# Kernel tuning notes

Hardware: AMD Instinct MI355X
Metric: run time of the kernel (lower is better)

The kernel has to match this reference:

```python
import jax, jax.numpy as jnp
import numpy as np

SZ = 256          # image side
K = 4             # neighbors
NUM_CHANNELS = 8
CHUNK = 512       # query chunk for brute-force KNN
BIG = 1e10        # penalty added to squared distance of non-filled candidates


def _fill_channel(img, mask):
    """img: [SZ,SZ] float, mask: [SZ,SZ] bool. Returns filled [SZ,SZ].

    Faithful to TreeMultiRandom: filled pixels = mask nonzero; for every
    unfilled pixel take K nearest filled pixels (Euclidean on coords/SZ,
    i.e. norm_coord) and fill with sum(val_j * dist_j) / sum(dist_j)
    (NOTE: the original weights by distance, not inverse distance; kept as-is).
    Filled pixels keep their (masked) value.
    """
    N = SZ * SZ
    r = jnp.arange(SZ, dtype=jnp.float32) / SZ  # norm_coord
    gy, gx = jnp.meshgrid(r, r, indexing='ij')  # (row, col) like .nonzero()
    py = gy.reshape(N)
    px = gx.reshape(N)
    mflat = mask.reshape(N)
    vflat = (img * mask).reshape(N)  # holed image values
    penalty = jnp.where(mflat, 0.0, BIG).astype(jnp.float32)

    def chunk_fn(q):
        qy, qx = q  # each [CHUNK]
        # masked squared distances to all candidates: [CHUNK, N]
        d2 = (qy[:, None] - py[None, :]) ** 2 + (qx[:, None] - px[None, :]) ** 2 \
             + penalty[None, :]
        neg, idx = jax.lax.top_k(-d2, K)          # K smallest distances
        dist = jnp.sqrt(jnp.maximum(-neg, 0.0))   # [CHUNK, K] (KDTree returns L2)
        v = vflat[idx]                            # gather neighbor values
        return jnp.sum(v * dist, axis=1) / jnp.sum(dist, axis=1)

    qys = py.reshape(-1, CHUNK)
    qxs = px.reshape(-1, CHUNK)
    vals = jax.lax.map(chunk_fn, (qys, qxs)).reshape(N)
    # unfilled pixels get interpolated vals; filled keep holed value
    return jnp.where(mflat, vflat, vals).reshape(SZ, SZ)


def reference(coded, lookup_table):
    img = coded[0, 0]  # [SZ, SZ]
    chans = [_fill_channel(img, lookup_table == c)
             for c in range(1, NUM_CHANNELS + 1)]
    return jnp.stack(chans)[None]  # [1, NUM_CHANNELS, SZ, SZ]


def setup_inputs() -> dict:
    key = jax.random.key(0)
    k1, k2 = jax.random.split(key)
    coded = jax.random.normal(k1, (1, 1, SZ, SZ), dtype=jnp.float32)
    # values in 1..NUM_CHANNELS so every channel has a nonempty filled set
    lookup_table = jax.random.randint(k2, (SZ, SZ), 1, NUM_CHANNELS + 1,
                                      dtype=jnp.int32)
    return {"coded": coded, "lookup_table": lookup_table}
```

## Files before the change

### kernel.cpp

```cpp
#include <hip/hip_runtime.h>
#include <math.h>

#define SZ 256
#define KNN 4
#define NUM_CHANNELS 8
#define R 7
#define WROWS (2 * R + 1)
#define RSTRIDE 6

typedef unsigned long long u64;
typedef unsigned int u32;

__device__ __forceinline__ void ins4(u32 key, u32& k0, u32& k1,
                                     u32& k2, u32& k3) {
    u32 m;
    m = (k2 > key) ? k2 : key;  k3 = (k3 < m) ? k3 : m;
    m = (k1 > key) ? k1 : key;  k2 = (k2 < m) ? k2 : m;
    m = (k0 > key) ? k0 : key;  k1 = (k1 < m) ? k1 : m;
    k0 = (k0 < key) ? k0 : key;
}

__device__ __forceinline__ void ins4_64(u64 key, u64& k0, u64& k1,
                                        u64& k2, u64& k3) {
    if (key < k3) {
        u64 m;
        m = (k2 > key) ? k2 : key;  k3 = (k3 < m) ? k3 : m;
        m = (k1 > key) ? k1 : key;  k2 = (k2 < m) ? k2 : m;
        m = (k0 > key) ? k0 : key;  k1 = (k1 < m) ? k1 : m;
        k0 = (k0 < key) ? k0 : key;
    }
}

__global__ __launch_bounds__(256) void knn_fill(
    const float* __restrict__ img,
    const int*   __restrict__ lut,
    float*       __restrict__ out)
{
    __shared__ u64 win[WROWS * RSTRIDE];

    const int x    = threadIdx.x;
    const int y    = blockIdx.x;
    const int ch   = blockIdx.y;
    const int c    = ch + 1;
    const int lane = x & 63;
    const int w64  = x >> 6;

    int y0 = y - R;
    if (y0 < 0) y0 = 0;
    if (y0 > SZ - WROWS) y0 = SZ - WROWS;

    if (x < WROWS * 2) win[(x >> 1) * RSTRIDE + (x & 1) * 5] = 0;

    #pragma unroll
    for (int rr = 0; rr < WROWS; ++rr) {
        const int v = lut[(y0 + rr) * SZ + x];
        const u64 bal = __ballot(v == c);
        if (lane == 0) win[rr * RSTRIDE + 1 + w64] = bal;
    }
    __syncthreads();

    const int pix = y * SZ + x;
    float* outc = out + (size_t)ch * (SZ * SZ);

    const int rrc = y - y0;
    if ((win[rrc * RSTRIDE + 1 + (x >> 6)] >> (x & 63)) & 1ull) {
        outc[pix] = img[pix];
        return;
    }

    u32 k0 = ~0u, k1 = ~0u, k2 = ~0u, k3 = ~0u;

    const int base = x - R + 64;
    const int wrd  = base >> 6;
    const int sh   = base & 63;

    #pragma unroll
    for (int rr = 0; rr < WROWS; ++rr) {
        const u64 lo = win[rr * RSTRIDE + wrd];
        const u64 hi = win[rr * RSTRIDE + wrd + 1];
        u32 w = (u32)((u64)(((((unsigned __int128)hi) << 64) | lo) >> sh))
                & ((1u << WROWS) - 1);
        const int dy   = y0 + rr - y;
        const int dy2  = dy * dy;
        const int rowx = (y0 + rr) * SZ + x;
        while (w) {
            const int b = __builtin_ctz(w);
            w &= w - 1;
            const int dx  = b - R;
            const u32 d2  = (u32)(dy2 + dx * dx);
            const u32 key = (d2 << 16) | (u32)(rowx + dx);
            ins4(key, k0, k1, k2, k3);
        }
    }

    u64 ks[KNN];
    const u32 in_d2 = k3 >> 16;
    if (in_d2 < (u32)((R + 1) * (R + 1))) {
        ks[0] = k0; ks[1] = k1; ks[2] = k2; ks[3] = k3;
    } else {
        const u64 cap = (in_d2 != 0xFFFFu) ? (u64)in_d2 : 65535ull;
        u64 q0 = ~0ull, q1 = ~0ull, q2 = ~0ull, q3 = ~0ull;
        for (int ady = 0; ady < SZ; ++ady) {
            u64 cur = q3 >> 16;
            if (cap < cur) cur = cap;
            const u64 a2 = (u64)(ady * ady);
            if (a2 > cur) break;
            int Rx;
            const u64 bound = cur - a2;
            if (bound >= 65025ull) Rx = SZ - 1;
            else Rx = (int)sqrtf((float)bound) + 1;
            int xs = x - Rx; if (xs < 0) xs = 0;
            int xe = x + Rx; if (xe > SZ - 1) xe = SZ - 1;
            for (int s = 0; s < 2; ++s) {
                if (s && ady == 0) continue;
                const int yy = s ? y + ady : y - ady;
                if (yy < 0 || yy > SZ - 1) continue;
                const int rb = yy * SZ;
                for (int xx = xs; xx <= xe; ++xx) {
                    if (lut[rb + xx] == c) {
                        const int dxx = xx - x;
                        const u64 d2 = a2 + (u64)(dxx * dxx);
                        ins4_64((d2 << 16) | (u32)(rb + xx), q0, q1, q2, q3);
                    }
                }
            }
        }
        ks[0] = q0; ks[1] = q1; ks[2] = q2; ks[3] = q3;
    }

    float num = 0.0f, den = 0.0f;
    #pragma unroll
    for (int i = 0; i < KNN; ++i) {
        const int idx = (int)(ks[i] & 0xFFFFull);
        const int d2i = (int)(ks[i] >> 16);
        const float dist = sqrtf((float)d2i * (1.0f / 65536.0f));
        num += img[idx] * dist;
        den += dist;
    }
    outc[pix] = num / den;
}

extern "C" void kernel_launch(void* const* d_in, const int* in_sizes, int n_in,
                              void* d_out, int out_size, void* d_ws, size_t ws_size,
                              hipStream_t stream) {
    const float* img = (const float*)d_in[0];
    const int*   lut = (const int*)d_in[1];
    float*       out = (float*)d_out;

    knn_fill<<<dim3(SZ, NUM_CHANNELS), dim3(256), 0, stream>>>(img, lut, out);
}
```

Baseline: 88.77 us.

## Widen shared bitmask window and scan fallback KNN with bitmask popcount iteration

Extends the shared-memory ballot bitmask window from 15 to 33 rows and rewrites the fallback search to walk set bits of the bitmask rather than reading the lookup table from global memory pixel by pixel. A third tier, the original global-memory scan, is kept for pixels whose fourth neighbor lies beyond radius 16. The aim is to cut global loads and the per-pixel loop cost for sparse channels. In exchange every block does more than twice as many ballot loads up front, even when the fallback never runs.

```diff
diff --git a/kernel.cpp b/kernel.cpp
--- a/kernel.cpp
+++ b/kernel.cpp
@@ -6,6 +6,8 @@
 #define NUM_CHANNELS 8
 #define R 7
 #define WROWS (2 * R + 1)
+#define FR 16
+#define FROWS (2 * FR + 1)
 #define RSTRIDE 6
 
 typedef unsigned long long u64;
@@ -36,7 +38,7 @@
     const int*   __restrict__ lut,
     float*       __restrict__ out)
 {
-    __shared__ u64 win[WROWS * RSTRIDE];
+    __shared__ u64 win[FROWS * RSTRIDE];
 
     const int x    = threadIdx.x;
     const int y    = blockIdx.x;
@@ -45,15 +47,19 @@
     const int lane = x & 63;
     const int w64  = x >> 6;
 
-    int y0 = y - R;
-    if (y0 < 0) y0 = 0;
-    if (y0 > SZ - WROWS) y0 = SZ - WROWS;
+    int y0b = y - FR;
+    if (y0b < 0) y0b = 0;
+    if (y0b > SZ - FROWS) y0b = SZ - FROWS;
+    int y0m = y - R;
+    if (y0m < 0) y0m = 0;
+    if (y0m > SZ - WROWS) y0m = SZ - WROWS;
+    const int rstart = y0m - y0b;
 
-    if (x < WROWS * 2) win[(x >> 1) * RSTRIDE + (x & 1) * 5] = 0;
+    if (x < FROWS * 2) win[(x >> 1) * RSTRIDE + (x & 1) * 5] = 0;
 
     #pragma unroll
-    for (int rr = 0; rr < WROWS; ++rr) {
-        const int v = lut[(y0 + rr) * SZ + x];
+    for (int rr = 0; rr < FROWS; ++rr) {
+        const int v = lut[(y0b + rr) * SZ + x];
         const u64 bal = __ballot(v == c);
         if (lane == 0) win[rr * RSTRIDE + 1 + w64] = bal;
     }
@@ -62,8 +68,7 @@
     const int pix = y * SZ + x;
     float* outc = out + (size_t)ch * (SZ * SZ);
 
-    const int rrc = y - y0;
-    if ((win[rrc * RSTRIDE + 1 + (x >> 6)] >> (x & 63)) & 1ull) {
+    if ((win[(y - y0b) * RSTRIDE + 1 + (x >> 6)] >> (x & 63)) & 1ull) {
         outc[pix] = img[pix];
         return;
     }
@@ -76,13 +81,14 @@
 
     #pragma unroll
     for (int rr = 0; rr < WROWS; ++rr) {
-        const u64 lo = win[rr * RSTRIDE + wrd];
-        const u64 hi = win[rr * RSTRIDE + wrd + 1];
+        const int rr2 = rstart + rr;
+        const u64 lo = win[rr2 * RSTRIDE + wrd];
+        const u64 hi = win[rr2 * RSTRIDE + wrd + 1];
         u32 w = (u32)((u64)(((((unsigned __int128)hi) << 64) | lo) >> sh))
                 & ((1u << WROWS) - 1);
-        const int dy   = y0 + rr - y;
+        const int dy   = y0m + rr - y;
         const int dy2  = dy * dy;
-        const int rowx = (y0 + rr) * SZ + x;
+        const int rowx = (y0m + rr) * SZ + x;
         while (w) {
             const int b = __builtin_ctz(w);
             w &= w - 1;
@@ -98,34 +104,76 @@
     if (in_d2 < (u32)((R + 1) * (R + 1))) {
         ks[0] = k0; ks[1] = k1; ks[2] = k2; ks[3] = k3;
     } else {
-        const u64 cap = (in_d2 != 0xFFFFu) ? (u64)in_d2 : 65535ull;
-        u64 q0 = ~0ull, q1 = ~0ull, q2 = ~0ull, q3 = ~0ull;
-        for (int ady = 0; ady < SZ; ++ady) {
-            u64 cur = q3 >> 16;
+        const u32 cap = in_d2;
+        u32 q0 = ~0u, q1 = ~0u, q2 = ~0u, q3 = ~0u;
+        for (int ady = 0; ady < FROWS; ++ady) {
+            u32 cur = q3 >> 16;
             if (cap < cur) cur = cap;
-            const u64 a2 = (u64)(ady * ady);
+            const u32 a2 = (u32)(ady * ady);
             if (a2 > cur) break;
-            int Rx;
-            const u64 bound = cur - a2;
-            if (bound >= 65025ull) Rx = SZ - 1;
-            else Rx = (int)sqrtf((float)bound) + 1;
+            const u32 bound = cur - a2;
+            int Rx = (bound >= 65025u) ? (SZ - 1)
+                                       : ((int)sqrtf((float)bound) + 1);
             int xs = x - Rx; if (xs < 0) xs = 0;
             int xe = x + Rx; if (xe > SZ - 1) xe = SZ - 1;
+            const int jxs = xs >> 6, jxe = xe >> 6;
+            const u64 mlo = (~0ull) << (xs & 63);
+            const u64 mhi = (~0ull) >> (63 - (xe & 63));
+            #pragma unroll
             for (int s = 0; s < 2; ++s) {
                 if (s && ady == 0) continue;
                 const int yy = s ? y + ady : y - ady;
-                if (yy < 0 || yy > SZ - 1) continue;
+                const int rr2 = yy - y0b;
+                if (rr2 < 0 || rr2 >= FROWS) continue;
                 const int rb = yy * SZ;
-                for (int xx = xs; xx <= xe; ++xx) {
-                    if (lut[rb + xx] == c) {
+                const u64* rw = &win[rr2 * RSTRIDE + 1];
+                for (int j = jxs; j <= jxe; ++j) {
+                    u64 w = rw[j];
+                    if (j == jxs) w &= mlo;
+                    if (j == jxe) w &= mhi;
+                    while (w) {
+                        const int b = __builtin_ctzll(w);
+                        w &= w - 1;
+                        const int xx = (j << 6) + b;
                         const int dxx = xx - x;
-                        const u64 d2 = a2 + (u64)(dxx * dxx);
-                        ins4_64((d2 << 16) | (u32)(rb + xx), q0, q1, q2, q3);
+                        const u32 d2 = a2 + (u32)(dxx * dxx);
+                        ins4((d2 << 16) | (u32)(rb + xx), q0, q1, q2, q3);
                     }
                 }
             }
         }
-        ks[0] = q0; ks[1] = q1; ks[2] = q2; ks[3] = q3;
+        if ((q3 >> 16) < 289u) {
+            ks[0] = q0; ks[1] = q1; ks[2] = q2; ks[3] = q3;
+        } else {
+            const u64 cap2 = (q3 != ~0u) ? (u64)(q3 >> 16) : (~0ull >> 16);
+            u64 t0 = ~0ull, t1 = ~0ull, t2 = ~0ull, t3 = ~0ull;
+            for (int ady = 0; ady < SZ; ++ady) {
+                u64 cur = t3 >> 16;
+                if (cap2 < cur) cur = cap2;
+                const u64 a2 = (u64)(ady * ady);
+                if (a2 > cur) break;
+                const u64 bound = cur - a2;
+                int Rx = (bound >= 65025ull) ? (SZ - 1)
+                                             : ((int)sqrtf((float)bound) + 1);
+                int xs = x - Rx; if (xs < 0) xs = 0;
+                int xe = x + Rx; if (xe > SZ - 1) xe = SZ - 1;
+                for (int s = 0; s < 2; ++s) {
+                    if (s && ady == 0) continue;
+                    const int yy = s ? y + ady : y - ady;
+                    if (yy < 0 || yy > SZ - 1) continue;
+                    const int rb = yy * SZ;
+                    for (int xx = xs; xx <= xe; ++xx) {
+                        if (lut[rb + xx] == c) {
+                            const int dxx = xx - x;
+                            const u64 d2 = a2 + (u64)(dxx * dxx);
+                            ins4_64((d2 << 16) | (u32)(rb + xx),
+                                    t0, t1, t2, t3);
+                        }
+                    }
+                }
+            }
+            ks[0] = t0; ks[1] = t1; ks[2] = t2; ks[3] = t3;
+        }
     }
 
     float num = 0.0f, den = 0.0f;
```

After: 79.09 us. -10.9%, faster.
